# Kernel optimization log

Hardware: AMD Instinct MI355X
Metric: run time of the kernel (lower is better)

Reference implementation:

```python
import jax, jax.numpy as jnp
import numpy as np

D = 768
H = 8
DH = D // H
SCALE = DH ** -0.5


def layer_norm(x, g, b, eps=1e-5):
    mu = jnp.mean(x, axis=-1, keepdims=True)
    var = jnp.var(x, axis=-1, keepdims=True)
    return (x - mu) * jax.lax.rsqrt(var + eps) * g + b


def setup_inputs() -> dict:
    key = jax.random.key(0)
    ks = jax.random.split(key, 8)
    B, N = 8, 1024
    s = lambda fan_in: 1.0 / np.sqrt(fan_in)
    return {
        "x": jax.random.normal(ks[0], (B, N, D), jnp.float32),
        "w_qkv": jax.random.normal(ks[1], (D, 3 * D), jnp.float32) * s(D),
        "w_o": jax.random.normal(ks[2], (D, D), jnp.float32) * s(D),
        "b_o": jnp.zeros((D,), jnp.float32),
        "w1": jax.random.normal(ks[3], (D, 4 * D), jnp.float32) * s(D),
        "b1": jnp.zeros((4 * D,), jnp.float32),
        "w2": jax.random.normal(ks[4], (4 * D, D), jnp.float32) * s(4 * D),
        "b2": jnp.zeros((D,), jnp.float32),
        "g1": jnp.ones((D,), jnp.float32), "be1": jnp.zeros((D,), jnp.float32),
        "gm": jnp.ones((D,), jnp.float32), "bm": jnp.zeros((D,), jnp.float32),
        "g3": jnp.ones((D,), jnp.float32), "be3": jnp.zeros((D,), jnp.float32),
    }


def reference(x, w_qkv, w_o, b_o, w1, b1, w2, b2, g1, be1, gm, bm, g3, be3):
    B, N, _ = x.shape
    # --- attention branch (pre-norm) ---
    h = layer_norm(x, g1, be1)
    qkv = h @ w_qkv                                   # (B,N,3D)
    qkv = qkv.reshape(B, N, 3, H, DH).transpose(2, 0, 3, 1, 4)  # (3,B,H,N,Dh)
    q, k, v = qkv[0], qkv[1], qkv[2]
    att = jax.nn.softmax(jnp.einsum('bhnd,bhmd->bhnm', q, k) * SCALE, axis=-1)
    o = jnp.einsum('bhnm,bhmd->bhnd', att, v)         # (B,H,N,Dh)
    # faithful to original: reshape WITHOUT transposing heads back
    o = o.reshape(B, N, D)
    o = o @ w_o + b_o
    x = o + x
    # --- MLP branch (has its own pre-norm; GELU after BOTH linears; dropout off) ---
    h = layer_norm(x, gm, bm)
    h = jax.nn.gelu(h @ w1 + b1, approximate=False)
    h = jax.nn.gelu(h @ w2 + b2, approximate=False)
    x = h + x
    return layer_norm(x, g3, be3)
```

## Files before the change

### kernel.cpp

```cpp
#include <hip/hip_runtime.h>
#include <cmath>
#include <cstdint>

typedef __bf16 bf16;
typedef __bf16 bf16x8 __attribute__((ext_vector_type(8)));
typedef __bf16 bf16x4 __attribute__((ext_vector_type(4)));
typedef float  f32x4  __attribute__((ext_vector_type(4)));

#define M_TOK 8192
#define SCALE_ 0.10206207261596575f
#define SB0 __builtin_amdgcn_sched_barrier(0)

__device__ __forceinline__ void gld_lds16(const void* g, void* l) {
  __builtin_amdgcn_global_load_lds(
      (__attribute__((address_space(1))) void*)(uintptr_t)g,
      (__attribute__((address_space(3))) void*)(uintptr_t)l,
      16, 0, 0);
}

__device__ __forceinline__ float gelu_f(float x) {
  float u = x * (0.7978845608f + 0.0356774081f * x * x);
  float t = 1.0f - 2.0f / (__expf(2.0f * u) + 1.0f);
  return 0.5f * x * (1.0f + t);
}

__global__ __launch_bounds__(256) void make_frags_kernel(
    const float* __restrict__ w_qkv, const float* __restrict__ w_o,
    const float* __restrict__ w1, const float* __restrict__ w2,
    bf16* __restrict__ fqkv, bf16* __restrict__ fwo, bf16* __restrict__ fw1,
    bf16* __restrict__ fw2) {
  int chunk = blockIdx.x * 4 + (threadIdx.x >> 6);
  int lane = threadIdx.x & 63;
  const float* src;
  bf16* dst;
  int K, N, base;
  if (chunk < 3456) {
    src = w_qkv; dst = fqkv; K = 768; N = 2304; base = 0;
  } else if (chunk < 4608) {
    src = w_o; dst = fwo; K = 768; N = 768; base = 3456;
  } else if (chunk < 9216) {
    src = w1; dst = fw1; K = 768; N = 3072; base = 4608;
  } else {
    src = w2; dst = fw2; K = 3072; N = 768; base = 9216;
  }
  int lid = chunk - base;
  int kc = K / 32;
  int n16 = lid / kc, c = lid - n16 * kc;
  int lr = lane & 15, qd = lane >> 4;
  int n = n16 * 16 + lr;
  int k0 = c * 32 + qd * 8;
  bf16x8 v;
#pragma unroll
  for (int e = 0; e < 8; e++) v[e] = (bf16)src[(size_t)(k0 + e) * N + n];
  *(bf16x8*)&dst[(size_t)lid * 512 + lane * 8] = v;
}

__global__ __launch_bounds__(256) void ln_kernel(
    const float* __restrict__ x, const float* __restrict__ g,
    const float* __restrict__ b, bf16* __restrict__ ob) {
  int w = threadIdx.x >> 6, lane = threadIdx.x & 63;
  size_t row = (size_t)blockIdx.x * 4 + w;
  const float* xr = x + row * 768;
  float4 v[3];
  float s = 0.f, sq = 0.f;
#pragma unroll
  for (int k = 0; k < 3; k++) {
    v[k] = *(const float4*)(xr + (k * 64 + lane) * 4);
    s += v[k].x + v[k].y + v[k].z + v[k].w;
    sq += v[k].x * v[k].x + v[k].y * v[k].y + v[k].z * v[k].z + v[k].w * v[k].w;
  }
#pragma unroll
  for (int off = 32; off >= 1; off >>= 1) {
    s += __shfl_xor(s, off);
    sq += __shfl_xor(sq, off);
  }
  float mean = s * (1.f / 768.f);
  float rstd = rsqrtf(sq * (1.f / 768.f) - mean * mean + 1e-5f);
#pragma unroll
  for (int k = 0; k < 3; k++) {
    int c = (k * 64 + lane) * 4;
    float4 gg = *(const float4*)(g + c);
    float4 bb = *(const float4*)(b + c);
    bf16x4 pk = {(bf16)((v[k].x - mean) * rstd * gg.x + bb.x),
                 (bf16)((v[k].y - mean) * rstd * gg.y + bb.y),
                 (bf16)((v[k].z - mean) * rstd * gg.z + bb.z),
                 (bf16)((v[k].w - mean) * rstd * gg.w + bb.w)};
    *(bf16x4*)(ob + row * 768 + c) = pk;
  }
}

__global__ __launch_bounds__(256) void ln3_reduce_kernel(
    const bf16* __restrict__ p, const float* __restrict__ b2,
    const bf16* __restrict__ x2, const float* __restrict__ g,
    const float* __restrict__ b, float* __restrict__ out) {
  int w = threadIdx.x >> 6, lane = threadIdx.x & 63;
  size_t row = (size_t)blockIdx.x * 4 + w;
  const bf16* p0 = p + row * 768;
  const bf16* p1 = p0 + (size_t)M_TOK * 768;
  const bf16* xr = x2 + row * 768;
  float4 v[3];
  float s = 0.f, sq = 0.f;
#pragma unroll
  for (int k = 0; k < 3; k++) {
    int c = (k * 64 + lane) * 4;
    bf16x4 a0 = *(const bf16x4*)(p0 + c);
    bf16x4 a1 = *(const bf16x4*)(p1 + c);
    float4 bb = *(const float4*)(b2 + c);
    bf16x4 rr = *(const bf16x4*)(xr + c);
    v[k].x = gelu_f((float)a0[0] + (float)a1[0] + bb.x) + (float)rr[0];
    v[k].y = gelu_f((float)a0[1] + (float)a1[1] + bb.y) + (float)rr[1];
    v[k].z = gelu_f((float)a0[2] + (float)a1[2] + bb.z) + (float)rr[2];
    v[k].w = gelu_f((float)a0[3] + (float)a1[3] + bb.w) + (float)rr[3];
    s += v[k].x + v[k].y + v[k].z + v[k].w;
    sq += v[k].x * v[k].x + v[k].y * v[k].y + v[k].z * v[k].z + v[k].w * v[k].w;
  }
#pragma unroll
  for (int off = 32; off >= 1; off >>= 1) {
    s += __shfl_xor(s, off);
    sq += __shfl_xor(sq, off);
  }
  float mean = s * (1.f / 768.f);
  float rstd = rsqrtf(sq * (1.f / 768.f) - mean * mean + 1e-5f);
#pragma unroll
  for (int k = 0; k < 3; k++) {
    int c = (k * 64 + lane) * 4;
    float4 gg = *(const float4*)(g + c);
    float4 bb = *(const float4*)(b + c);
    float4 ov = {(v[k].x - mean) * rstd * gg.x + bb.x,
                 (v[k].y - mean) * rstd * gg.y + bb.y,
                 (v[k].z - mean) * rstd * gg.z + bb.z,
                 (v[k].w - mean) * rstd * gg.w + bb.w};
    *(float4*)(out + row * 768 + c) = ov;
  }
}

template <int EPI, int LDA, int KTOT, int KSL, int NN>
__global__ __launch_bounds__(256, 3) void gemm128_kernel(
    const bf16* __restrict__ A, const bf16* __restrict__ Bf,
    const float* __restrict__ bias, bf16* __restrict__ outb,
    bf16* __restrict__ qo, bf16* __restrict__ ko, bf16* __restrict__ vto) {
  constexpr int KCg = KTOT / 32;
  constexpr int NT = KSL / 32;
  __shared__ __align__(16) bf16 smem[3][8192];
  int tid = threadIdx.x;
  int w = tid >> 6, l = tid & 63;
  int qd = l >> 4, lr = l & 15;
  int id2 = blockIdx.y * gridDim.x + blockIdx.x;
  int xcd = id2 & 7;
  int slot = id2 >> 3;
  int Mg = gridDim.x >> 3;
  int mt = xcd * Mg + (slot % Mg);
  int ntl = slot / Mg;
  int bm0 = mt * 128, bn0 = ntl * 128;
  int kb = blockIdx.z * KSL;
  int wm = (w >> 1) * 64, wn = (w & 1) * 64;
  int wnl = (w & 1) * 4;

  const bf16* pA = A + (size_t)(bm0 + w * 32 + (l >> 2)) * LDA + kb +
                   (((l & 3) ^ ((l >> 3) & 3)) * 8);
  const bf16* pB =
      Bf + ((size_t)((bn0 >> 4) + w * 2) * KCg + (kb >> 5)) * 512 + l * 8;

  auto STG = [&](int t, int b) {
    char* dA = (char*)smem[b] + w * 2048;
    char* dB = (char*)smem[b] + 8192 + w * 2048;
    gld_lds16(pA + t * 32, dA);
    gld_lds16(pA + t * 32 + (size_t)16 * LDA, dA + 1024);
    gld_lds16(pB + (size_t)t * 512, dB);
    gld_lds16(pB + (size_t)KCg * 512 + (size_t)t * 512, dB + 1024);
  };
  auto LDF = [&](int b, bf16x8* af, bf16x8* bv) {
    const bf16* Ab = smem[b];
    const bf16* Bb = smem[b] + 4096;
#pragma unroll
    for (int i = 0; i < 4; ++i) {
      int r = wm + i * 16 + lr;
      af[i] = *(const bf16x8*)(Ab + r * 32 + ((qd ^ ((lr >> 1) & 3)) * 8));
    }
#pragma unroll
    for (int j = 0; j < 4; ++j)
      bv[j] = *(const bf16x8*)(Bb + (wnl + j) * 512 + l * 8);
  };

  f32x4 acc[4][4] = {};

  STG(0, 0);
  STG(1, 1);
  asm volatile("s_waitcnt vmcnt(4)" ::: "memory");
  SB0;
  __builtin_amdgcn_s_barrier();

#pragma unroll 1
  for (int t3 = 0; t3 < NT; t3 += 3) {
#pragma unroll
    for (int u = 0; u < 3; ++u) {
      const int t = t3 + u;
      const bool st = (t + 2) < NT;
      if (st) STG(t + 2, (u + 2) % 3);
      SB0;
      bf16x8 af[4], bv[4];
      LDF(u, af, bv);
      asm volatile("s_waitcnt lgkmcnt(0)" ::: "memory");
      SB0;
      __builtin_amdgcn_s_setprio(1);
#pragma unroll
      for (int i = 0; i < 4; ++i)
#pragma unroll
        for (int j = 0; j < 4; ++j)
          acc[i][j] = __builtin_amdgcn_mfma_f32_16x16x32_bf16(
              af[i], bv[j], acc[i][j], 0, 0, 0);
      __builtin_amdgcn_s_setprio(0);
      if (t + 1 < NT) {
        if (st) asm volatile("s_waitcnt vmcnt(4)" ::: "memory");
        else    asm volatile("s_waitcnt vmcnt(0)" ::: "memory");
        SB0;
        __builtin_amdgcn_s_barrier();
      }
    }
  }

  bf16* outbs = (EPI == 5) ? outb + (size_t)blockIdx.z * M_TOK * NN : outb;

#pragma unroll
  for (int i = 0; i < 4; i++) {
#pragma unroll
    for (int j = 0; j < 4; j++) {
      if (EPI == 4) {
        int colt = bn0 + wn + j * 16;
        int which = colt / 768;
        int rem = colt - which * 768;
        int h = rem / 96;
        int dhb = rem - h * 96;
        int row0 = bm0 + wm + i * 16 + qd * 4;
        int b = row0 >> 10, n0 = row0 & 1023;
        int bh = b * 8 + h;
        if (which == 2) {
          bf16x4 pk = {(bf16)acc[i][j][0], (bf16)acc[i][j][1],
                       (bf16)acc[i][j][2], (bf16)acc[i][j][3]};
          *(bf16x4*)(vto + ((size_t)(bh * 96 + dhb + lr)) * 1024 + n0) = pk;
        } else if (which == 0) {
#pragma unroll
          for (int r = 0; r < 4; r++)
            qo[((size_t)bh * 1024 + n0 + r) * 96 + dhb + lr] =
                (bf16)(acc[i][j][r] * SCALE_);
        } else {
#pragma unroll
          for (int r = 0; r < 4; r++)
            ko[((size_t)bh * 1024 + n0 + r) * 96 + dhb + lr] =
                (bf16)acc[i][j][r];
        }
      } else {
#pragma unroll
        for (int r = 0; r < 4; r++) {
          int row = bm0 + wm + i * 16 + qd * 4 + r;
          int col = bn0 + wn + j * 16 + lr;
          size_t o = (size_t)row * NN + col;
          float v = acc[i][j][r];
          if (EPI == 2) {
            outbs[o] = (bf16)gelu_f(v + bias[col]);
          } else {
            outbs[o] = (bf16)v;
          }
        }
      }
    }
  }
}

__global__ __launch_bounds__(256) void attn_kernel(
    const bf16* __restrict__ qb, const bf16* __restrict__ kb,
    const bf16* __restrict__ vtb, const bf16* __restrict__ fwo,
    const float* __restrict__ bo, const float* __restrict__ xres,
    const float* __restrict__ gm, const float* __restrict__ bm,
    bf16* __restrict__ x2o, bf16* __restrict__ h2o) {
  __shared__ __align__(16) bf16 Ks[2][64 * 104];
  __shared__ __align__(16) bf16 Vs[2][96 * 72];
  __shared__ __align__(16) bf16 Ps[128 * 72];
  int t = threadIdx.x;
  int w = t >> 6, lane = t & 63;
  int qd = lane >> 4, lr = lane & 15;
  int bh = blockIdx.x, nt0 = blockIdx.y * 128;
  int bq = bh >> 3, hh = bh & 7;

  const bf16* kgb = kb + (size_t)bh * 1024 * 96;
  const bf16* vgb = vtb + (size_t)bh * 96 * 1024;

  bf16x8 kreg[3], vreg[3];
#pragma unroll
  for (int it = 0; it < 3; it++) {
    int idx = it * 256 + t;
    kreg[it] = *(const bf16x8*)(kgb + (idx / 12) * 96 + (idx % 12) * 8);
    vreg[it] = *(const bf16x8*)(vgb + (size_t)(idx >> 3) * 1024 + (idx & 7) * 8);
  }

  const bf16* qg = qb + ((size_t)bh * 1024 + nt0 + w * 32) * 96;
  bf16x8 afq[2][3];
#pragma unroll
  for (int i = 0; i < 2; i++)
#pragma unroll
    for (int ks = 0; ks < 3; ks++)
      afq[i][ks] = *(const bf16x8*)(qg + (i * 16 + lr) * 96 + ks * 32 + qd * 8);

  f32x4 oacc[2][6] = {};
  float lst[2][4] = {};

  int cur = 0;
  for (int kt = 0; kt < 16; kt++) {
#pragma unroll
    for (int it = 0; it < 3; it++) {
      int idx = it * 256 + t;
      *(bf16x8*)&Ks[cur][(idx / 12) * 104 + (idx % 12) * 8] = kreg[it];
      *(bf16x8*)&Vs[cur][(idx >> 3) * 72 + (idx & 7) * 8] = vreg[it];
    }
    if (kt < 15) {
      const bf16* kg = kgb + (size_t)(kt + 1) * 64 * 96;
      const bf16* vg = vgb + (kt + 1) * 64;
#pragma unroll
      for (int it = 0; it < 3; it++) {
        int idx = it * 256 + t;
        kreg[it] = *(const bf16x8*)(kg + (idx / 12) * 96 + (idx % 12) * 8);
        vreg[it] =
            *(const bf16x8*)(vg + (size_t)(idx >> 3) * 1024 + (idx & 7) * 8);
      }
    }
    __syncthreads();

    f32x4 sacc[2][4] = {};
#pragma unroll
    for (int ks = 0; ks < 3; ks++) {
      bf16x8 bk[4];
#pragma unroll
      for (int jn = 0; jn < 4; jn++)
        bk[jn] =
            *(const bf16x8*)&Ks[cur][(jn * 16 + lr) * 104 + ks * 32 + qd * 8];
#pragma unroll
      for (int i = 0; i < 2; i++)
#pragma unroll
        for (int jn = 0; jn < 4; jn++)
          sacc[i][jn] = __builtin_amdgcn_mfma_f32_16x16x32_bf16(
              afq[i][ks], bk[jn], sacc[i][jn], 0, 0, 0);
    }

#pragma unroll
    for (int i = 0; i < 2; i++)
#pragma unroll
      for (int jn = 0; jn < 4; jn++)
#pragma unroll
        for (int r = 0; r < 4; r++) {
          float p = __expf(sacc[i][jn][r]);
          lst[i][r] += p;
          Ps[(w * 32 + i * 16 + qd * 4 + r) * 72 + ((jn ^ qd) * 16 + lr)] =
              (bf16)p;
        }

#pragma unroll
    for (int ks = 0; ks < 2; ks++) {
      bf16x8 ap[2];
#pragma unroll
      for (int i = 0; i < 2; i++)
        ap[i] = *(const bf16x8*)&Ps[(w * 32 + i * 16 + lr) * 72 +
                                    ((ks * 32 + qd * 8) ^
                                     (((lr >> 2) & 3) * 16))];
#pragma unroll
      for (int jn = 0; jn < 6; jn++) {
        bf16x8 bv =
            *(const bf16x8*)&Vs[cur][(jn * 16 + lr) * 72 + ks * 32 + qd * 8];
#pragma unroll
        for (int i = 0; i < 2; i++)
          oacc[i][jn] = __builtin_amdgcn_mfma_f32_16x16x32_bf16(
              ap[i], bv, oacc[i][jn], 0, 0, 0);
      }
    }
    cur ^= 1;
  }

#pragma unroll
  for (int i = 0; i < 2; i++)
#pragma unroll
    for (int r = 0; r < 4; r++) {
#pragma unroll
      for (int off = 1; off < 16; off <<= 1)
        lst[i][r] += __shfl_xor(lst[i][r], off);
    }

  bf16* Po = (bf16*)&Ks[0][0];
  float* red = (float*)&Vs[0][0];
  int Rbase = bq * 1024 + hh * 128 + (nt0 >> 3);

  __syncthreads();
#pragma unroll
  for (int i = 0; i < 2; i++) {
#pragma unroll
    for (int r = 0; r < 4; r++) {
      float inv = 1.0f / lst[i][r];
      int nn = i * 16 + qd * 4 + r;
      int rloc = w * 4 + (nn >> 3);
      int colb = 96 * (nn & 7);
#pragma unroll
      for (int jn = 0; jn < 6; jn++)
        Po[rloc * 784 + colb + jn * 16 + lr] = (bf16)(oacc[i][jn][r] * inv);
    }
  }
  __syncthreads();

  f32x4 ya[12] = {};
#pragma unroll 1
  for (int kc = 0; kc < 24; ++kc) {
    bf16x8 a = *(const bf16x8*)&Po[lr * 784 + kc * 32 + qd * 8];
    const bf16* bp = fwo + ((size_t)(w * 12) * 24 + kc) * 512 + lane * 8;
#pragma unroll
    for (int j = 0; j < 12; ++j)
      ya[j] = __builtin_amdgcn_mfma_f32_16x16x32_bf16(
          a, *(const bf16x8*)(bp + (size_t)j * 12288), ya[j], 0, 0, 0);
  }

  float s4[4] = {}, q4[4] = {};
#pragma unroll
  for (int j = 0; j < 12; ++j) {
    int col = (w * 12 + j) * 16 + lr;
    float bcol = bo[col];
#pragma unroll
    for (int rr = 0; rr < 4; ++rr) {
      size_t R = (size_t)(Rbase + qd * 4 + rr);
      float tv = ya[j][rr] + bcol + xres[R * 768 + col];
      ya[j][rr] = tv;
      s4[rr] += tv;
      q4[rr] += tv * tv;
    }
  }
#pragma unroll
  for (int rr = 0; rr < 4; ++rr) {
#pragma unroll
    for (int off = 1; off < 16; off <<= 1) {
      s4[rr] += __shfl_xor(s4[rr], off);
      q4[rr] += __shfl_xor(q4[rr], off);
    }
  }
  if (lr == 0) {
#pragma unroll
    for (int rr = 0; rr < 4; ++rr) {
      red[(qd * 4 + rr) * 8 + w * 2] = s4[rr];
      red[(qd * 4 + rr) * 8 + w * 2 + 1] = q4[rr];
    }
  }
  __syncthreads();
  float mean[4], rstd[4];
#pragma unroll
  for (int rr = 0; rr < 4; ++rr) {
    float ss = 0.f, qq = 0.f;
#pragma unroll
    for (int wv = 0; wv < 4; ++wv) {
      ss += red[(qd * 4 + rr) * 8 + wv * 2];
      qq += red[(qd * 4 + rr) * 8 + wv * 2 + 1];
    }
    mean[rr] = ss * (1.f / 768.f);
    rstd[rr] = rsqrtf(qq * (1.f / 768.f) - mean[rr] * mean[rr] + 1e-5f);
  }
#pragma unroll
  for (int j = 0; j < 12; ++j) {
    int col = (w * 12 + j) * 16 + lr;
    float gg = gm[col], bb = bm[col];
#pragma unroll
    for (int rr = 0; rr < 4; ++rr) {
      size_t R = (size_t)(Rbase + qd * 4 + rr);
      float tv = ya[j][rr];
      x2o[R * 768 + col] = (bf16)tv;
      h2o[R * 768 + col] = (bf16)((tv - mean[rr]) * rstd[rr] * gg + bb);
    }
  }
}

extern "C" void kernel_launch(void* const* d_in, const int* in_sizes, int n_in,
                              void* d_out, int out_size, void* d_ws,
                              size_t ws_size, hipStream_t stream) {
  const float* x = (const float*)d_in[0];
  const float* w_qkv = (const float*)d_in[1];
  const float* w_o = (const float*)d_in[2];
  const float* b_o = (const float*)d_in[3];
  const float* w1 = (const float*)d_in[4];
  const float* b1 = (const float*)d_in[5];
  const float* w2 = (const float*)d_in[6];
  const float* b2 = (const float*)d_in[7];
  const float* g1 = (const float*)d_in[8];
  const float* be1 = (const float*)d_in[9];
  const float* gm = (const float*)d_in[10];
  const float* bm = (const float*)d_in[11];
  const float* g3 = (const float*)d_in[12];
  const float* be3 = (const float*)d_in[13];

  char* ws = (char*)d_ws;
  size_t off = 0;
  auto alloc = [&](size_t bytes) {
    char* p = ws + off;
    off += (bytes + 255) & ~(size_t)255;
    return p;
  };
  const size_t SZ_TOK_BF = (size_t)M_TOK * 768 * 2;
  bf16* fqkv = (bf16*)alloc((size_t)2304 * 768 * 2);
  bf16* fwo = (bf16*)alloc((size_t)768 * 768 * 2);
  bf16* fw1 = (bf16*)alloc((size_t)3072 * 768 * 2);
  bf16* fw2 = (bf16*)alloc((size_t)768 * 3072 * 2);
  bf16* hA = (bf16*)alloc(SZ_TOK_BF);
  bf16* qb = (bf16*)alloc(SZ_TOK_BF);
  bf16* kbuf = (bf16*)alloc(SZ_TOK_BF);
  bf16* vtb = (bf16*)alloc(SZ_TOK_BF);
  bf16* x2 = (bf16*)alloc(SZ_TOK_BF);
  char* G = alloc((size_t)M_TOK * 3072 * 2);
  bf16* h2 = hA;
  bf16* a1 = (bf16*)G;
  bf16* pW2 = hA;

  make_frags_kernel<<<3456, 256, 0, stream>>>(w_qkv, w_o, w1, w2, fqkv, fwo,
                                              fw1, fw2);

  ln_kernel<<<M_TOK / 4, 256, 0, stream>>>(x, g1, be1, hA);

  gemm128_kernel<4, 768, 768, 768, 2304><<<dim3(64, 18), 256, 0, stream>>>(
      hA, fqkv, nullptr, nullptr, qb, kbuf, vtb);

  attn_kernel<<<dim3(64, 8), 256, 0, stream>>>(qb, kbuf, vtb, fwo, b_o, x, gm,
                                               bm, x2, h2);

  gemm128_kernel<2, 768, 768, 768, 3072><<<dim3(64, 24), 256, 0, stream>>>(
      h2, fw1, b1, a1, nullptr, nullptr, nullptr);

  gemm128_kernel<5, 3072, 3072, 1536, 768><<<dim3(64, 6, 2), 256, 0, stream>>>(
      a1, fw2, nullptr, pW2, nullptr, nullptr, nullptr);

  ln3_reduce_kernel<<<M_TOK / 4, 256, 0, stream>>>(pW2, b2, x2, g3, be3,
                                                   (float*)d_out);
}
```

Baseline: 319.0 us.

## Double attention block to 256 queries with 512 threads sharing K/V tiles

The attention kernel now runs 8 waves per block, covering 256 query rows instead of 128, so each staged K/V tile in LDS is reused by twice as many waves and total K/V global traffic is halved. The fused output projection is retiled so each wave computes two 16-row groups over 6 column tiles, which reuses each w_o fragment load for two MFMAs. The LayerNorm reduction is extended to 8 waves. The grid halves to 256 blocks and LDS grows to about 89 KB with launch bounds of one block per CU, so occupancy and load balance across CUs may suffer.

```diff
diff --git a/kernel.cpp b/kernel.cpp
--- a/kernel.cpp
+++ b/kernel.cpp
@@ -267,30 +267,36 @@
   }
 }
 
-__global__ __launch_bounds__(256) void attn_kernel(
+__global__ __launch_bounds__(512, 1) void attn_kernel(
     const bf16* __restrict__ qb, const bf16* __restrict__ kb,
     const bf16* __restrict__ vtb, const bf16* __restrict__ fwo,
     const float* __restrict__ bo, const float* __restrict__ xres,
     const float* __restrict__ gm, const float* __restrict__ bm,
     bf16* __restrict__ x2o, bf16* __restrict__ h2o) {
-  __shared__ __align__(16) bf16 Ks[2][64 * 104];
-  __shared__ __align__(16) bf16 Vs[2][96 * 72];
-  __shared__ __align__(16) bf16 Ps[128 * 72];
+  __shared__ __align__(16) char lds_raw[91136];
+  bf16* const KsB = (bf16*)lds_raw;
+  bf16* const VsB = (bf16*)(lds_raw + 26624);
+  bf16* const Ps = (bf16*)(lds_raw + 54272);
   int t = threadIdx.x;
   int w = t >> 6, lane = t & 63;
   int qd = lane >> 4, lr = lane & 15;
-  int bh = blockIdx.x, nt0 = blockIdx.y * 128;
+  int bh = blockIdx.x, nt0 = blockIdx.y * 256;
   int bq = bh >> 3, hh = bh & 7;
 
   const bf16* kgb = kb + (size_t)bh * 1024 * 96;
   const bf16* vgb = vtb + (size_t)bh * 96 * 1024;
 
-  bf16x8 kreg[3], vreg[3];
+  bf16x8 sreg[3];
 #pragma unroll
   for (int it = 0; it < 3; it++) {
-    int idx = it * 256 + t;
-    kreg[it] = *(const bf16x8*)(kgb + (idx / 12) * 96 + (idx % 12) * 8);
-    vreg[it] = *(const bf16x8*)(vgb + (size_t)(idx >> 3) * 1024 + (idx & 7) * 8);
+    int c = it * 512 + t;
+    if (c < 768) {
+      sreg[it] = *(const bf16x8*)(kgb + (c / 12) * 96 + (c % 12) * 8);
+    } else {
+      int cv = c - 768;
+      sreg[it] =
+          *(const bf16x8*)(vgb + (size_t)(cv >> 3) * 1024 + (cv & 7) * 8);
+    }
   }
 
   const bf16* qg = qb + ((size_t)bh * 1024 + nt0 + w * 32) * 96;
@@ -306,21 +312,31 @@
 
   int cur = 0;
   for (int kt = 0; kt < 16; kt++) {
+    bf16* Ksc = KsB + cur * 6656;
+    bf16* Vsc = VsB + cur * 6912;
 #pragma unroll
     for (int it = 0; it < 3; it++) {
-      int idx = it * 256 + t;
-      *(bf16x8*)&Ks[cur][(idx / 12) * 104 + (idx % 12) * 8] = kreg[it];
-      *(bf16x8*)&Vs[cur][(idx >> 3) * 72 + (idx & 7) * 8] = vreg[it];
+      int c = it * 512 + t;
+      if (c < 768) {
+        *(bf16x8*)&Ksc[(c / 12) * 104 + (c % 12) * 8] = sreg[it];
+      } else {
+        int cv = c - 768;
+        *(bf16x8*)&Vsc[(cv >> 3) * 72 + (cv & 7) * 8] = sreg[it];
+      }
     }
     if (kt < 15) {
       const bf16* kg = kgb + (size_t)(kt + 1) * 64 * 96;
       const bf16* vg = vgb + (kt + 1) * 64;
 #pragma unroll
       for (int it = 0; it < 3; it++) {
-        int idx = it * 256 + t;
-        kreg[it] = *(const bf16x8*)(kg + (idx / 12) * 96 + (idx % 12) * 8);
-        vreg[it] =
-            *(const bf16x8*)(vg + (size_t)(idx >> 3) * 1024 + (idx & 7) * 8);
+        int c = it * 512 + t;
+        if (c < 768) {
+          sreg[it] = *(const bf16x8*)(kg + (c / 12) * 96 + (c % 12) * 8);
+        } else {
+          int cv = c - 768;
+          sreg[it] =
+              *(const bf16x8*)(vg + (size_t)(cv >> 3) * 1024 + (cv & 7) * 8);
+        }
       }
     }
     __syncthreads();
@@ -332,7 +348,7 @@
 #pragma unroll
       for (int jn = 0; jn < 4; jn++)
         bk[jn] =
-            *(const bf16x8*)&Ks[cur][(jn * 16 + lr) * 104 + ks * 32 + qd * 8];
+            *(const bf16x8*)&Ksc[(jn * 16 + lr) * 104 + ks * 32 + qd * 8];
 #pragma unroll
       for (int i = 0; i < 2; i++)
 #pragma unroll
@@ -364,7 +380,7 @@
 #pragma unroll
       for (int jn = 0; jn < 6; jn++) {
         bf16x8 bv =
-            *(const bf16x8*)&Vs[cur][(jn * 16 + lr) * 72 + ks * 32 + qd * 8];
+            *(const bf16x8*)&Vsc[(jn * 16 + lr) * 72 + ks * 32 + qd * 8];
 #pragma unroll
         for (int i = 0; i < 2; i++)
           oacc[i][jn] = __builtin_amdgcn_mfma_f32_16x16x32_bf16(
@@ -383,8 +399,8 @@
         lst[i][r] += __shfl_xor(lst[i][r], off);
     }
 
-  bf16* Po = (bf16*)&Ks[0][0];
-  float* red = (float*)&Vs[0][0];
+  bf16* Po = (bf16*)lds_raw;
+  float* red = (float*)(lds_raw + 54272);
   int Rbase = bq * 1024 + hh * 128 + (nt0 >> 3);
 
   __syncthreads();
@@ -393,80 +409,99 @@
 #pragma unroll
     for (int r = 0; r < 4; r++) {
       float inv = 1.0f / lst[i][r];
-      int nn = i * 16 + qd * 4 + r;
-      int rloc = w * 4 + (nn >> 3);
+      int nn = w * 32 + i * 16 + qd * 4 + r;
+      int rloc = nn >> 3;
       int colb = 96 * (nn & 7);
 #pragma unroll
       for (int jn = 0; jn < 6; jn++)
-        Po[rloc * 784 + colb + jn * 16 + lr] = (bf16)(oacc[i][jn][r] * inv);
+        Po[rloc * 792 + colb + jn * 16 + lr] = (bf16)(oacc[i][jn][r] * inv);
     }
   }
   __syncthreads();
 
-  f32x4 ya[12] = {};
-#pragma unroll 1
+  f32x4 ya[2][6] = {};
+#pragma unroll 2
   for (int kc = 0; kc < 24; ++kc) {
-    bf16x8 a = *(const bf16x8*)&Po[lr * 784 + kc * 32 + qd * 8];
-    const bf16* bp = fwo + ((size_t)(w * 12) * 24 + kc) * 512 + lane * 8;
-#pragma unroll
-    for (int j = 0; j < 12; ++j)
-      ya[j] = __builtin_amdgcn_mfma_f32_16x16x32_bf16(
-          a, *(const bf16x8*)(bp + (size_t)j * 12288), ya[j], 0, 0, 0);
-  }
-
-  float s4[4] = {}, q4[4] = {};
-#pragma unroll
-  for (int j = 0; j < 12; ++j) {
-    int col = (w * 12 + j) * 16 + lr;
+    bf16x8 a0 = *(const bf16x8*)&Po[lr * 792 + kc * 32 + qd * 8];
+    bf16x8 a1 = *(const bf16x8*)&Po[(16 + lr) * 792 + kc * 32 + qd * 8];
+    const bf16* bp = fwo + ((size_t)(w * 6) * 24 + kc) * 512 + lane * 8;
+#pragma unroll
+    for (int j = 0; j < 6; ++j) {
+      bf16x8 bv = *(const bf16x8*)(bp + (size_t)j * 12288);
+      ya[0][j] = __builtin_amdgcn_mfma_f32_16x16x32_bf16(a0, bv, ya[0][j], 0,
+                                                         0, 0);
+      ya[1][j] = __builtin_amdgcn_mfma_f32_16x16x32_bf16(a1, bv, ya[1][j], 0,
+                                                         0, 0);
+    }
+  }
+
+  float s4[2][4] = {}, q4[2][4] = {};
+#pragma unroll
+  for (int j = 0; j < 6; ++j) {
+    int col = (w * 6 + j) * 16 + lr;
     float bcol = bo[col];
 #pragma unroll
+    for (int g = 0; g < 2; ++g)
+#pragma unroll
+      for (int rr = 0; rr < 4; ++rr) {
+        size_t R = (size_t)(Rbase + g * 16 + qd * 4 + rr);
+        float tv = ya[g][j][rr] + bcol + xres[R * 768 + col];
+        ya[g][j][rr] = tv;
+        s4[g][rr] += tv;
+        q4[g][rr] += tv * tv;
+      }
+  }
+#pragma unroll
+  for (int g = 0; g < 2; ++g)
+#pragma unroll
     for (int rr = 0; rr < 4; ++rr) {
-      size_t R = (size_t)(Rbase + qd * 4 + rr);
-      float tv = ya[j][rr] + bcol + xres[R * 768 + col];
-      ya[j][rr] = tv;
-      s4[rr] += tv;
-      q4[rr] += tv * tv;
-    }
-  }
-#pragma unroll
-  for (int rr = 0; rr < 4; ++rr) {
-#pragma unroll
-    for (int off = 1; off < 16; off <<= 1) {
-      s4[rr] += __shfl_xor(s4[rr], off);
-      q4[rr] += __shfl_xor(q4[rr], off);
-    }
-  }
+#pragma unroll
+      for (int off = 1; off < 16; off <<= 1) {
+        s4[g][rr] += __shfl_xor(s4[g][rr], off);
+        q4[g][rr] += __shfl_xor(q4[g][rr], off);
+      }
+    }
   if (lr == 0) {
 #pragma unroll
+    for (int g = 0; g < 2; ++g)
+#pragma unroll
+      for (int rr = 0; rr < 4; ++rr) {
+        int rloc = g * 16 + qd * 4 + rr;
+        red[rloc * 16 + w * 2] = s4[g][rr];
+        red[rloc * 16 + w * 2 + 1] = q4[g][rr];
+      }
+  }
+  __syncthreads();
+  float mean[2][4], rstd[2][4];
+#pragma unroll
+  for (int g = 0; g < 2; ++g)
+#pragma unroll
     for (int rr = 0; rr < 4; ++rr) {
-      red[(qd * 4 + rr) * 8 + w * 2] = s4[rr];
-      red[(qd * 4 + rr) * 8 + w * 2 + 1] = q4[rr];
-    }
-  }
-  __syncthreads();
-  float mean[4], rstd[4];
-#pragma unroll
-  for (int rr = 0; rr < 4; ++rr) {
-    float ss = 0.f, qq = 0.f;
-#pragma unroll
-    for (int wv = 0; wv < 4; ++wv) {
-      ss += red[(qd * 4 + rr) * 8 + wv * 2];
-      qq += red[(qd * 4 + rr) * 8 + wv * 2 + 1];
-    }
-    mean[rr] = ss * (1.f / 768.f);
-    rstd[rr] = rsqrtf(qq * (1.f / 768.f) - mean[rr] * mean[rr] + 1e-5f);
-  }
-#pragma unroll
-  for (int j = 0; j < 12; ++j) {
-    int col = (w * 12 + j) * 16 + lr;
+      int rloc = g * 16 + qd * 4 + rr;
+      float ss = 0.f, qq = 0.f;
+#pragma unroll
+      for (int wv = 0; wv < 8; ++wv) {
+        ss += red[rloc * 16 + wv * 2];
+        qq += red[rloc * 16 + wv * 2 + 1];
+      }
+      mean[g][rr] = ss * (1.f / 768.f);
+      rstd[g][rr] =
+          rsqrtf(qq * (1.f / 768.f) - mean[g][rr] * mean[g][rr] + 1e-5f);
+    }
+#pragma unroll
+  for (int j = 0; j < 6; ++j) {
+    int col = (w * 6 + j) * 16 + lr;
     float gg = gm[col], bb = bm[col];
 #pragma unroll
-    for (int rr = 0; rr < 4; ++rr) {
-      size_t R = (size_t)(Rbase + qd * 4 + rr);
-      float tv = ya[j][rr];
-      x2o[R * 768 + col] = (bf16)tv;
-      h2o[R * 768 + col] = (bf16)((tv - mean[rr]) * rstd[rr] * gg + bb);
-    }
+    for (int g = 0; g < 2; ++g)
+#pragma unroll
+      for (int rr = 0; rr < 4; ++rr) {
+        size_t R = (size_t)(Rbase + g * 16 + qd * 4 + rr);
+        float tv = ya[g][j][rr];
+        x2o[R * 768 + col] = (bf16)tv;
+        h2o[R * 768 + col] =
+            (bf16)((tv - mean[g][rr]) * rstd[g][rr] * gg + bb);
+      }
   }
 }
 
@@ -518,7 +553,7 @@
   gemm128_kernel<4, 768, 768, 768, 2304><<<dim3(64, 18), 256, 0, stream>>>(
       hA, fqkv, nullptr, nullptr, qb, kbuf, vtb);
 
-  attn_kernel<<<dim3(64, 8), 256, 0, stream>>>(qb, kbuf, vtb, fwo, b_o, x, gm,
+  attn_kernel<<<dim3(64, 4), 512, 0, stream>>>(qb, kbuf, vtb, fwo, b_o, x, gm,
                                                bm, x2, h2);
 
   gemm128_kernel<2, 768, 768, 768, 3072><<<dim3(64, 24), 256, 0, stream>>>(
```

Measured after the change: 327.8 us. 2.7% more time.
